# Optimization experiments

Measured on AMD Instinct MI355X. Metric: run time of the kernel, lower is better.

Reference implementation:

```python
import jax, jax.numpy as jnp
import numpy as np

TIME_TOL = 0.1      # Time_tolerance for the BEFORE temporal relation
DECAY = 0.8         # decay_rate of the Hawkes-style kernel
RES = 0.03          # integral_resolution
# body-predicate incidence: BODY[h, p] = 1 if predicate p appears in the body of head h's formula
BODY = jnp.array([[0.0, 1.0, 1.0], [1.0, 0.0, 0.0], [1.0, 0.0, 0.0]], dtype=jnp.float32)


def setup_inputs() -> dict:
    key = jax.random.key(0)
    k1, k2, k3, k4 = jax.random.split(key, 4)
    S, P, E = 64, 3, 128
    T_max = 50
    event_times = jnp.sort(jax.random.uniform(k1, (S, P, E), dtype=jnp.float32) * T_max, axis=-1)
    event_mask = jax.random.randint(k2, (S, P, E), 0, 2).astype(jnp.float32)
    base = jax.random.uniform(k3, (P,), dtype=jnp.float32) * 0.3 + 0.1
    weight = jax.random.uniform(k4, (P,), dtype=jnp.float32) * 0.5 + 0.1
    return {"event_times": event_times, "event_mask": event_mask, "base": base, "weight": weight, "T_max": T_max}


def _final_intensity(raw, base):
    # if raw >= 0: max(raw, base) else exp(raw)  (matches the .item() branching in intensity())
    return jnp.where(raw >= 0.0, jnp.maximum(raw, base), jnp.exp(raw))


def reference(event_times, event_mask, base, weight, T_max):
    dtype = event_times.dtype
    grid = jnp.asarray(np.arange(0.0, float(T_max), RES), dtype=dtype)  # [G]
    body = BODY.astype(dtype)
    # ---- integral term: intensity on the fine grid ----
    diff_g = grid[None, None, :, None] - event_times[:, :, None, :]          # [S,P,G,E]
    k_g = jnp.sum(jnp.exp(-DECAY * jnp.maximum(diff_g, 0.0))
                  * (diff_g > TIME_TOL) * event_mask[:, :, None, :], axis=-1)  # [S,P,G]
    feat_g = jnp.einsum('hp,spg->shg', body, k_g)                            # [S,H,G]
    lam_g = _final_intensity(base[None, :, None] + weight[None, :, None] * feat_g,
                             base[None, :, None])
    integral = jnp.sum(lam_g) * RES
    # ---- log-sum term: intensity at each head's own event times (skip first event) ----
    diff_q = event_times[:, :, :, None, None] - event_times[:, None, None, :, :]  # [S,H,Eq,P,E]
    k_q = jnp.sum(jnp.exp(-DECAY * jnp.maximum(diff_q, 0.0))
                  * (diff_q > TIME_TOL) * event_mask[:, None, None, :, :], axis=-1)  # [S,H,Eq,P]
    feat_q = jnp.einsum('hp,shep->she', body, k_q)                           # [S,H,Eq]
    lam_q = _final_intensity(base[None, :, None] + weight[None, :, None] * feat_q,
                             base[None, :, None])
    E = event_times.shape[-1]
    valid_q = event_mask * (jnp.arange(E) >= 1)  # transitions skip the first event, honor padding mask
    log_sum = jnp.sum(jnp.where(valid_q > 0, jnp.log(lam_q), 0.0))
    return log_sum - integral
```

## Files before the change

kernel.cpp:

```cpp
#include <hip/hip_runtime.h>


#define PP 3
#define EE 128
#define GXB 8

__device__ __forceinline__ float wave_sum(float v) {
#pragma unroll
    for (int o = 32; o > 0; o >>= 1) v += __shfl_down(v, o, 64);
    return v;
}

__device__ __forceinline__ int bsearch_cnt(const float* __restrict__ pt, float t) {
    int lo = 0, hi = EE;
#pragma unroll
    for (int it = 0; it < 7; ++it) {
        int mid = (lo + hi) >> 1;
        if (lo < hi) {
            if (t - pt[mid] > 0.1f) lo = mid + 1; else hi = mid;
        }
    }
    return lo;
}

__global__ void __launch_bounds__(256)
hawkes_ll_kernel(const float* __restrict__ et, const float* __restrict__ em,
                 const float* __restrict__ base, const float* __restrict__ weight,
                 const int* __restrict__ tmax_p, float* __restrict__ out)
{
    __shared__ float s_et[PP * EE];
    __shared__ float s_em[PP * EE];
    __shared__ float s_pref[PP][EE + 1];
    __shared__ float s_red[4];

    const int s   = blockIdx.y;
    const int bx  = blockIdx.x;
    const int tid = threadIdx.x;
    const int lane = tid & 63;
    const int wv   = tid >> 6;

    const size_t boff = (size_t)s * PP * EE;
    for (int i = tid; i < PP * EE; i += 256) {
        s_et[i] = et[boff + i];
        s_em[i] = em[boff + i];
    }
    __syncthreads();

    if (wv < PP) {
        const int p = wv;
        float x0 = s_em[p * EE + lane] * __expf(0.8f * s_et[p * EE + lane]);
#pragma unroll
        for (int o = 1; o < 64; o <<= 1) {
            float y = __shfl_up(x0, o, 64);
            if (lane >= o) x0 += y;
        }
        float tot0 = __shfl(x0, 63, 64);
        float x1 = s_em[p * EE + 64 + lane] * __expf(0.8f * s_et[p * EE + 64 + lane]);
#pragma unroll
        for (int o = 1; o < 64; o <<= 1) {
            float y = __shfl_up(x1, o, 64);
            if (lane >= o) x1 += y;
        }
        x1 += tot0;
        if (lane == 0) s_pref[p][0] = 0.0f;
        s_pref[p][lane + 1] = x0;
        s_pref[p][64 + lane + 1] = x1;
    }
    __syncthreads();

    const int tmax = *tmax_p;
    const int G = (int)ceil((double)tmax / 0.03);
    const float b0 = base[0], b1 = base[1], b2 = base[2];
    const float w0 = weight[0], w1 = weight[1], w2 = weight[2];
    const float bsum = b0 + b1 + b2;
    const float w12 = w1 + w2;

    float val = 0.0f;

    for (int g = bx * 256 + tid; g < G; g += GXB * 256) {
        const float t = (float)((double)g * 0.03);
        const float decay = __expf(-0.8f * t);
        const float k0 = decay * s_pref[0][bsearch_cnt(s_et + 0 * EE, t)];
        const float k1 = decay * s_pref[1][bsearch_cnt(s_et + 1 * EE, t)];
        const float k2 = decay * s_pref[2][bsearch_cnt(s_et + 2 * EE, t)];
        val -= 0.03f * (bsum + w0 * (k1 + k2) + w12 * k0);
    }

    if (bx == 0) {
        for (int i = tid; i < PP * EE; i += 256) {
            const int h  = i >> 7;
            const int eq = i & (EE - 1);
            const float tq = s_et[h * EE + eq];
            const float decay = __expf(-0.8f * tq);
            const float k0 = decay * s_pref[0][bsearch_cnt(s_et + 0 * EE, tq)];
            const float k1 = decay * s_pref[1][bsearch_cnt(s_et + 1 * EE, tq)];
            const float k2 = decay * s_pref[2][bsearch_cnt(s_et + 2 * EE, tq)];
            const float feat = (h == 0) ? (k1 + k2) : k0;
            const float bh = (h == 0) ? b0 : ((h == 1) ? b1 : b2);
            const float wh = (h == 0) ? w0 : ((h == 1) ? w1 : w2);
            const float lam = bh + wh * feat;
            if (eq >= 1 && s_em[h * EE + eq] > 0.0f) val += __logf(lam);
        }
    }

    float r = wave_sum(val);
    if (lane == 0) s_red[wv] = r;
    __syncthreads();
    if (tid == 0) {
        float tot = s_red[0] + s_red[1] + s_red[2] + s_red[3];
        atomicAdd(out, tot);
    }
}

extern "C" void kernel_launch(void* const* d_in, const int* in_sizes, int n_in,
                              void* d_out, int out_size, void* d_ws, size_t ws_size,
                              hipStream_t stream) {
    const float* et     = (const float*)d_in[0];
    const float* em     = (const float*)d_in[1];
    const float* base   = (const float*)d_in[2];
    const float* weight = (const float*)d_in[3];
    const int*   tmax   = (const int*)d_in[4];
    float* out = (float*)d_out;

    const int S = in_sizes[0] / (PP * EE);

    hipMemsetAsync(out, 0, sizeof(float) * out_size, stream);

    dim3 grid(GXB, S);
    hawkes_ll_kernel<<<grid, 256, 0, stream>>>(et, em, base, weight, tmax, out);
}
```

Baseline: 70.02 us.

## Replace grid integral with closed-form geometric sums per event

```diff
diff --git a/kernel.cpp b/kernel.cpp
--- a/kernel.cpp
+++ b/kernel.cpp
@@ -3,7 +3,6 @@
 
 #define PP 3
 #define EE 128
-#define GXB 8
 
 __device__ __forceinline__ float wave_sum(float v) {
 #pragma unroll
@@ -24,20 +23,17 @@
 }
 
 __global__ void __launch_bounds__(256)
-hawkes_ll_kernel(const float* __restrict__ et, const float* __restrict__ em,
-                 const float* __restrict__ base, const float* __restrict__ weight,
-                 const int* __restrict__ tmax_p, float* __restrict__ out)
+hawkes_main(const float* __restrict__ et, const float* __restrict__ em,
+            const float* __restrict__ base, const float* __restrict__ weight,
+            const int* __restrict__ tmax_p, float* __restrict__ partials)
 {
     __shared__ float s_et[PP * EE];
     __shared__ float s_em[PP * EE];
     __shared__ float s_pref[PP][EE + 1];
     __shared__ float s_red[4];
 
-    const int s   = blockIdx.y;
-    const int bx  = blockIdx.x;
-    const int tid = threadIdx.x;
-    const int lane = tid & 63;
-    const int wv   = tid >> 6;
+    const int s = blockIdx.y, bx = blockIdx.x, tid = threadIdx.x;
+    const int lane = tid & 63, wv = tid >> 6;
 
     const size_t boff = (size_t)s * PP * EE;
     for (int i = tid; i < PP * EE; i += 256) {
@@ -72,43 +68,68 @@
     const int G = (int)ceil((double)tmax / 0.03);
     const float b0 = base[0], b1 = base[1], b2 = base[2];
     const float w0 = weight[0], w1 = weight[1], w2 = weight[2];
-    const float bsum = b0 + b1 + b2;
     const float w12 = w1 + w2;
 
     float val = 0.0f;
+    const int i = bx * 256 + tid;
 
-    for (int g = bx * 256 + tid; g < G; g += GXB * 256) {
-        const float t = (float)((double)g * 0.03);
-        const float decay = __expf(-0.8f * t);
-        const float k0 = decay * s_pref[0][bsearch_cnt(s_et + 0 * EE, t)];
-        const float k1 = decay * s_pref[1][bsearch_cnt(s_et + 1 * EE, t)];
-        const float k2 = decay * s_pref[2][bsearch_cnt(s_et + 2 * EE, t)];
-        val -= 0.03f * (bsum + w0 * (k1 + k2) + w12 * k0);
-    }
-
-    if (bx == 0) {
-        for (int i = tid; i < PP * EE; i += 256) {
-            const int h  = i >> 7;
-            const int eq = i & (EE - 1);
-            const float tq = s_et[h * EE + eq];
-            const float decay = __expf(-0.8f * tq);
-            const float k0 = decay * s_pref[0][bsearch_cnt(s_et + 0 * EE, tq)];
-            const float k1 = decay * s_pref[1][bsearch_cnt(s_et + 1 * EE, tq)];
-            const float k2 = decay * s_pref[2][bsearch_cnt(s_et + 2 * EE, tq)];
-            const float feat = (h == 0) ? (k1 + k2) : k0;
-            const float bh = (h == 0) ? b0 : ((h == 1) ? b1 : b2);
-            const float wh = (h == 0) ? w0 : ((h == 1) ? w1 : w2);
-            const float lam = bh + wh * feat;
-            if (eq >= 1 && s_em[h * EE + eq] > 0.0f) val += __logf(lam);
+    if (i < PP * EE) {
+        const int p = i >> 7;
+        const float m = s_em[i];
+        if (m > 0.0f) {
+            const float te = s_et[i];
+            int g0 = (int)(((double)te + 0.1) / 0.03) - 2;
+            if (g0 < 0) g0 = 0;
+            while (g0 < G && !((float)((double)g0 * 0.03) - te > 0.1f)) ++g0;
+            if (g0 < G) {
+                const float d0 = (float)((double)g0 * 0.03) - te;
+                const float r = __expf(-0.024f);
+                const float inv1mr = 1.0f / (1.0f - r);
+                const float rn = __expf(-0.024f * (float)(G - g0));
+                const float gsum = __expf(-0.8f * d0) * (1.0f - rn) * inv1mr;
+                const float cp = (p == 0) ? w12 : w0;
+                val -= 0.03f * cp * gsum;
+            }
         }
+    } else {
+        const int j = i - PP * EE;
+        const int h = j >> 7, eq = j & (EE - 1);
+        const float tq = s_et[j];
+        const float decay = __expf(-0.8f * tq);
+        const float k0 = decay * s_pref[0][bsearch_cnt(s_et + 0 * EE, tq)];
+        const float k1 = decay * s_pref[1][bsearch_cnt(s_et + 1 * EE, tq)];
+        const float k2 = decay * s_pref[2][bsearch_cnt(s_et + 2 * EE, tq)];
+        const float feat = (h == 0) ? (k1 + k2) : k0;
+        const float bh = (h == 0) ? b0 : ((h == 1) ? b1 : b2);
+        const float wh = (h == 0) ? w0 : ((h == 1) ? w1 : w2);
+        if (eq >= 1 && s_em[j] > 0.0f) val += __logf(bh + wh * feat);
     }
 
     float r = wave_sum(val);
     if (lane == 0) s_red[wv] = r;
     __syncthreads();
+    if (tid == 0)
+        partials[blockIdx.y * gridDim.x + bx] = s_red[0] + s_red[1] + s_red[2] + s_red[3];
+}
+
+__global__ void __launch_bounds__(256)
+hawkes_reduce(const float* __restrict__ partials, int n,
+              const float* __restrict__ base, const int* __restrict__ tmax_p,
+              float* __restrict__ out, int S)
+{
+    __shared__ float s_red[4];
+    const int tid = threadIdx.x;
+    float v = 0.0f;
+    for (int i = tid; i < n; i += 256) v += partials[i];
+    float r = wave_sum(v);
+    if ((tid & 63) == 0) s_red[tid >> 6] = r;
+    __syncthreads();
     if (tid == 0) {
-        float tot = s_red[0] + s_red[1] + s_red[2] + s_red[3];
-        atomicAdd(out, tot);
+        const int tmax = *tmax_p;
+        const int G = (int)ceil((double)tmax / 0.03);
+        const float bsum = base[0] + base[1] + base[2];
+        out[0] = (s_red[0] + s_red[1] + s_red[2] + s_red[3])
+                 - 0.03f * (float)S * (float)G * bsum;
     }
 }
 
@@ -121,11 +142,12 @@
     const float* weight = (const float*)d_in[3];
     const int*   tmax   = (const int*)d_in[4];
     float* out = (float*)d_out;
+    float* partials = (float*)d_ws;
 
     const int S = in_sizes[0] / (PP * EE);
+    const int GX = 3;
 
-    hipMemsetAsync(out, 0, sizeof(float) * out_size, stream);
-
-    dim3 grid(GXB, S);
-    hawkes_ll_kernel<<<grid, 256, 0, stream>>>(et, em, base, weight, tmax, out);
+    dim3 grid(GX, S);
+    hawkes_main<<<grid, 256, 0, stream>>>(et, em, base, weight, tmax, partials);
+    hawkes_reduce<<<1, 256, 0, stream>>>(partials, GX * S, base, tmax, out, S);
 }
```

Measured after the change: 65.29 us. 1.07x faster.
